# Kernel tuning notes

Measured on AMD Instinct MI355X. Metric: run time of the kernel, lower is better.

The kernel has to match this reference:

```python
import jax, jax.numpy as jnp
import numpy as np


def _dct1d_last(x, W_r, W_i):
    """DCT-II along last axis via the even/odd-reorder + FFT trick, ortho norm.

    x: [..., N] real. W_r/W_i: [1, N] rows = cos/sin(-k*pi/(2N)).
    """
    N = x.shape[-1]
    # v = [x[0], x[2], ...] ++ [x[N-1], x[N-3], ..., x[1]]  (torch index/inverted_index)
    v = jnp.concatenate([x[..., 0::2], x[..., 1::2][..., ::-1]], axis=-1)
    Vc = jnp.fft.fft(v, axis=-1)  # complex64
    V = Vc.real * W_r - Vc.imag * W_i  # [..., N]
    # ortho normalization: V[0] /= sqrt(N)*2 ; V[1:] /= sqrt(N/2)*2 ; then V *= 2
    s0 = 1.0 / (np.sqrt(N) * 2.0)
    s1 = 1.0 / (np.sqrt(N / 2.0) * 2.0)
    scale = jnp.concatenate([jnp.full((1,), s0, x.dtype), jnp.full((N - 1,), s1, x.dtype)])
    return 2.0 * V * scale


def setup_inputs() -> dict:
    key = jax.random.key(0)
    H, W = 512, 512
    x = jax.random.normal(key, (32, 3, H, W), dtype=jnp.float32)
    kw = -jnp.arange(W, dtype=jnp.float32)[None, :] * np.pi / (2 * W)
    kh = -jnp.arange(H, dtype=jnp.float32)[None, :] * np.pi / (2 * H)
    return {
        "x": x,
        "W_r_weight": jnp.cos(kw), "W_i_weight": jnp.sin(kw),
        "W_r_height": jnp.cos(kh), "W_i_height": jnp.sin(kh),
    }


def reference(x, W_r_weight, W_i_weight, W_r_height, W_i_height):
    # DCT along width (last axis)
    V = _dct1d_last(x, W_r_weight, W_i_weight)
    # transpose last two dims, DCT along height, transpose back
    V = jnp.swapaxes(V, -1, -2)
    V = _dct1d_last(V, W_r_height, W_i_height)
    return jnp.swapaxes(V, -1, -2)
```

## Files before the change

kernel.cpp:

```cpp
#include <hip/hip_runtime.h>
#include <math.h>

#define NN 512

typedef __attribute__((ext_vector_type(8))) short bf16x8;
typedef __attribute__((ext_vector_type(4))) float f32x4;
typedef __attribute__((ext_vector_type(4))) unsigned int u32x4;

__device__ inline unsigned short f2bf(float f) {
    unsigned u = __builtin_bit_cast(unsigned, f);
    u += 0x7fffu + ((u >> 16) & 1u);
    return (unsigned short)(u >> 16);
}
__device__ inline float bf2f(unsigned short h) {
    unsigned u = ((unsigned)h) << 16;
    return __builtin_bit_cast(float, u);
}
__device__ inline unsigned cvtpk_bf16(float lo, float hi) {
    unsigned r;
    asm("v_cvt_pk_bf16_f32 %0, %1, %2" : "=v"(r) : "v"(lo), "v"(hi));
    return r;
}

__global__ __launch_bounds__(256) void fill_dct_half(unsigned short* __restrict__ Ce,
                                                     unsigned short* __restrict__ Co) {
    int idx = blockIdx.x * 256 + threadIdx.x;
    int par = idx >> 16;
    int kk = (idx >> 8) & 255;
    int n = idx & 255;
    int k = 2 * kk + par;
    int m = ((2 * n + 1) * k) & 2047;
    float ang = (float)m * 3.0679615757712823e-3f;
    float s = (k == 0) ? 0.04419417382415922f : 0.0625f;
    unsigned short v = f2bf(s * cosf(ang));
    if (par) Co[kk * 256 + n] = v; else Ce[kk * 256 + n] = v;
}

#define GLB(p) ((const __attribute__((address_space(1))) unsigned int*)(const void*)(p))
#define LDS(p) ((__attribute__((address_space(3))) unsigned int*)(p))

template <int PASS>
__global__ __launch_bounds__(512, 4) void gemm_dct(const void* __restrict__ Ap,
                                                   const unsigned short* __restrict__ Ce,
                                                   const unsigned short* __restrict__ Cop,
                                                   void* __restrict__ Outp,
                                                   size_t strideIn, size_t strideOut) {
    const int nwg = (int)gridDim.x;
    const int cpx = nwg >> 3;
    const int bid = (int)blockIdx.x;
    const int nid = (bid & 7) * cpx + (bid >> 3);
    const int bx = nid & 3;
    const int by = (nid >> 2) & 3;
    const int bz = nid >> 4;

    __shared__ unsigned short sm[PASS == 1 ? 37376 : 20480];
    unsigned short* const As = sm;
    unsigned short* const Bs = sm + (PASS == 1 ? 8192 : 12288);
    unsigned short* const Rs = (PASS == 1) ? As : Bs;
    unsigned short* const Gs = (PASS == 1) ? Bs : As;
    unsigned short* const smE = sm + 20480;

    const int t = threadIdx.x;
    const int lane = t & 63;
    const int wave = t >> 6;
    const int wr = wave >> 2, wc = wave & 3;
    const int lr = lane & 15;
    const int kgx = ((lane >> 4) * 8) ^ (((lr >> 1) & 3) << 3);

    const int srow = t >> 2;
    const int sslot = t & 3;
    const int scol = (sslot ^ ((srow >> 1) & 3)) * 8;

    const int frow = t >> 2;
    const int fq = t & 3;
    const int fslot = (fq ^ ((frow >> 1) & 3)) * 8;

    const float* Xf = nullptr;
    const unsigned short* Tp = nullptr;
    const unsigned short* Gmat;
    int grow0, sgn, row0, col0;
    if constexpr (PASS == 1) {
        Xf = (const float*)Ap + (size_t)bz * strideIn;
        row0 = by * 128;
        col0 = bx * 128;
        Gmat = (bx < 2) ? Ce : Cop; grow0 = (bx & 1) * 128; sgn = (bx >= 2);
    } else {
        Tp = (const unsigned short*)Ap + (size_t)bz * strideIn;
        col0 = bx * 128;
        row0 = 0;
        Gmat = (by < 2) ? Ce : Cop; grow0 = (by & 1) * 128; sgn = (by >= 2);
    }
    const float sgnf = sgn ? -1.0f : 1.0f;

    f32x4 acc[4][2] = {};

    f32x4 rfA[2], rmA[2], rfB[2], rmB[2];
    bf16x8 gfA, gmA, gfB, gmB;

    auto stageG = [&](int buf, int k0) {
        __builtin_amdgcn_global_load_lds(GLB(Gmat + (size_t)(grow0 + srow) * 256 + k0 + scol),
                                         LDS(&Gs[buf * 4096 + srow * 32 + sslot * 8]), 16, 0, 0);
    };
    auto lr1 = [&](f32x4 (&rf)[2], f32x4 (&rm)[2], int k0) {
        const float* bfp = Xf + (size_t)(row0 + frow) * NN + k0 + fq * 8;
        const float* bmp = Xf + (size_t)(row0 + frow) * NN + (504 - k0 - fq * 8);
        rf[0] = *reinterpret_cast<const f32x4*>(bfp);
        rf[1] = *reinterpret_cast<const f32x4*>(bfp + 4);
        rm[0] = *reinterpret_cast<const f32x4*>(bmp);
        rm[1] = *reinterpret_cast<const f32x4*>(bmp + 4);
    };
    auto cw1 = [&](f32x4 (&rf)[2], f32x4 (&rm)[2], int buf) {
        unsigned p[4];
#pragma unroll
        for (int q = 0; q < 4; ++q) {
            const int j0 = 2 * q, j1 = 2 * q + 1;
            const int r0 = 7 - j0, r1 = 7 - j1;
            float s0 = fmaf(sgnf, rm[r0 >> 2][r0 & 3], rf[j0 >> 2][j0 & 3]);
            float s1 = fmaf(sgnf, rm[r1 >> 2][r1 & 3], rf[j1 >> 2][j1 & 3]);
            p[q] = cvtpk_bf16(s0, s1);
        }
        u32x4 w = {p[0], p[1], p[2], p[3]};
        *reinterpret_cast<u32x4*>(&Rs[buf * 4096 + frow * 32 + fslot]) = w;
    };
    auto lr2 = [&](bf16x8& gf, bf16x8& gm, int k0) {
        const unsigned short* bfp = Tp + (size_t)(col0 + frow) * NN + k0 + fq * 8;
        const unsigned short* bmp = Tp + (size_t)(col0 + frow) * NN + (504 - k0 - fq * 8);
        gf = *reinterpret_cast<const bf16x8*>(bfp);
        gm = *reinterpret_cast<const bf16x8*>(bmp);
    };
    auto cw2 = [&](bf16x8& gf, bf16x8& gm, int buf) {
        unsigned p[4];
#pragma unroll
        for (int q = 0; q < 4; ++q) {
            const int j0 = 2 * q, j1 = 2 * q + 1;
            float a0 = bf2f((unsigned short)gf[j0]);
            float a1 = bf2f((unsigned short)gf[j1]);
            float b0 = bf2f((unsigned short)gm[7 - j0]);
            float b1 = bf2f((unsigned short)gm[7 - j1]);
            p[q] = cvtpk_bf16(fmaf(sgnf, b0, a0), fmaf(sgnf, b1, a1));
        }
        u32x4 w = {p[0], p[1], p[2], p[3]};
        *reinterpret_cast<u32x4*>(&Rs[buf * 4096 + frow * 32 + fslot]) = w;
    };
    auto compute = [&](int kt) {
        const int rofs = (kt & 1) * 4096;
        const int gofs = (kt % 3) * 4096;
        const int aofs = (PASS == 1) ? rofs : gofs;
        const int bofs = (PASS == 1) ? gofs : rofs;
        bf16x8 a[4], b[2];
#pragma unroll
        for (int mi = 0; mi < 4; ++mi)
            a[mi] = *reinterpret_cast<const bf16x8*>(
                &As[aofs + (wr * 64 + mi * 16 + lr) * 32 + kgx]);
#pragma unroll
        for (int ni = 0; ni < 2; ++ni)
            b[ni] = *reinterpret_cast<const bf16x8*>(
                &Bs[bofs + (wc * 32 + ni * 16 + lr) * 32 + kgx]);
        __builtin_amdgcn_s_setprio(1);
#pragma unroll
        for (int mi = 0; mi < 4; ++mi)
#pragma unroll
            for (int ni = 0; ni < 2; ++ni)
                acc[mi][ni] = __builtin_amdgcn_mfma_f32_16x16x32_bf16(a[mi], b[ni],
                                                                      acc[mi][ni], 0, 0, 0);
        __builtin_amdgcn_s_setprio(0);
    };
    auto doLR = [&](int s, int k0) {
        if constexpr (PASS == 1) {
            if (s & 1) lr1(rfB, rmB, k0); else lr1(rfA, rmA, k0);
        } else {
            if (s & 1) lr2(gfB, gmB, k0); else lr2(gfA, gmA, k0);
        }
    };
    auto doCW = [&](int s) {
        const int buf = s & 1;
        if constexpr (PASS == 1) {
            if (s & 1) cw1(rfB, rmB, buf); else cw1(rfA, rmA, buf);
        } else {
            if (s & 1) cw2(gfB, gmB, buf); else cw2(gfA, gmA, buf);
        }
    };

    stageG(0, 0);
    doLR(0, 0);
    asm volatile("" ::: "memory");
    doCW(0);
    stageG(1, 32);
    asm volatile("" ::: "memory");
    doLR(1, 32);
    doLR(2, 64);
    asm volatile("s_waitcnt lgkmcnt(0)" ::: "memory");
    if constexpr (PASS == 1) asm volatile("s_waitcnt vmcnt(8)" ::: "memory");
    else                     asm volatile("s_waitcnt vmcnt(4)" ::: "memory");
    __builtin_amdgcn_s_barrier();

#pragma unroll
    for (int kt = 0; kt < 8; ++kt) {
        if (kt + 1 <= 7) doCW(kt + 1);
        if (kt + 2 <= 7) stageG((kt + 2) % 3, (kt + 2) * 32);
        asm volatile("" ::: "memory");
        if (kt + 3 <= 7) doLR(kt + 3, (kt + 3) * 32);
        compute(kt);
        asm volatile("s_waitcnt lgkmcnt(0)" ::: "memory");
        if (kt <= 4) {
            if constexpr (PASS == 1) asm volatile("s_waitcnt vmcnt(9)" ::: "memory");
            else                     asm volatile("s_waitcnt vmcnt(5)" ::: "memory");
        } else if (kt == 5) {
            if constexpr (PASS == 1) asm volatile("s_waitcnt vmcnt(5)" ::: "memory");
            else                     asm volatile("s_waitcnt vmcnt(3)" ::: "memory");
        } else if (kt == 6) {
            asm volatile("s_waitcnt vmcnt(0)" ::: "memory");
        }
        if (kt < 7) __builtin_amdgcn_s_barrier();
    }

    if constexpr (PASS == 1) {
        unsigned short* T = (unsigned short*)Outp + (size_t)bz * strideOut;
#pragma unroll
        for (int mi = 0; mi < 4; ++mi)
#pragma unroll
            for (int ni = 0; ni < 2; ++ni) {
                int gr = wr * 64 + mi * 16 + (lane >> 4) * 4;
                int gc = wc * 32 + ni * 16 + lr;
                ushort4 v;
                v.x = f2bf(acc[mi][ni][0]);
                v.y = f2bf(acc[mi][ni][1]);
                v.z = f2bf(acc[mi][ni][2]);
                v.w = f2bf(acc[mi][ni][3]);
                *reinterpret_cast<ushort4*>(&smE[gc * 132 + gr]) = v;
            }
        asm volatile("s_waitcnt lgkmcnt(0)" ::: "memory");
        __builtin_amdgcn_s_barrier();
#pragma unroll
        for (int it = 0; it < 4; ++it) {
            int gcr = wave * 16 + it * 4 + (lane >> 4);
            int physRow = (bx & 1) * 256 + 2 * gcr + (bx >> 1);
            int cb = lr * 8;
            u32x4 d = *reinterpret_cast<const u32x4*>(&smE[gcr * 132 + cb]);
            *reinterpret_cast<u32x4*>(&T[(size_t)physRow * NN + row0 + cb]) = d;
        }
    } else {
        float* O = (float*)Outp + (size_t)bz * strideOut;
#pragma unroll
        for (int mi = 0; mi < 4; ++mi)
#pragma unroll
            for (int ni = 0; ni < 2; ++ni) {
                int gc = col0 + wc * 32 + ni * 16 + lr;
#pragma unroll
                for (int rr = 0; rr < 4; ++rr) {
                    int grl = wr * 64 + mi * 16 + (lane >> 4) * 4 + rr;
                    int ih = (by & 1) * 128 + grl;
                    int q = 2 * ih + (by >> 1);
                    O[(size_t)q * NN + gc] = acc[mi][ni][rr];
                }
            }
    }
}

extern "C" void kernel_launch(void* const* d_in, const int* in_sizes, int n_in,
                              void* d_out, int out_size, void* d_ws, size_t ws_size,
                              hipStream_t stream) {
    const float* x = (const float*)d_in[0];
    float* out = (float*)d_out;

    const int imgs = in_sizes[0] / (NN * NN);
    const size_t imgElems = (size_t)NN * NN;
    const size_t imgB16 = imgElems * 2;

    unsigned short* Ce = (unsigned short*)d_ws;
    unsigned short* Co = Ce + 65536;
    unsigned short* Tb = Co + 65536;

    long long budget = (long long)ws_size - 262144;
    int maxchunk = (int)(budget / (long long)imgB16);
    if (maxchunk < 1) maxchunk = 1;
    if (maxchunk > imgs) maxchunk = imgs;

    hipLaunchKernelGGL(fill_dct_half, dim3(512), dim3(256), 0, stream, Ce, Co);

    for (int i0 = 0; i0 < imgs; i0 += maxchunk) {
        int c = imgs - i0 < maxchunk ? imgs - i0 : maxchunk;
        hipLaunchKernelGGL((gemm_dct<1>), dim3(16 * c), dim3(512), 0, stream,
                           x + (size_t)i0 * imgElems, Ce, Co, Tb, imgElems, imgElems);
        hipLaunchKernelGGL((gemm_dct<2>), dim3(16 * c), dim3(512), 0, stream,
                           Tb, Ce, Co, out + (size_t)i0 * imgElems, imgElems, imgElems);
    }
}
```

Measured before the change: 74.77 us.

## Enlarge GEMM tiles to 128x256 per block and halve the grid

Each workgroup now computes a 128x256 output tile: it stages a full 256-row half of the DCT basis (even or odd parity) and fuses the parity into the block index. Each wave moves from a 4x2 to a 4x4 MFMA accumulator grid, so more math is done per LDS fragment load. Every block now serves both 128-column halves of its parity, so the fold of the input row is loaded and formed once instead of twice. The register prefetch depth drops from two stages to one and the wait counts are adjusted to match. The costs are more accumulator registers, a larger LDS footprint that may reduce occupancy, half as many blocks for the GPU to spread across its compute units, and less latency hiding on the global loads.

```diff
diff --git a/kernel.cpp b/kernel.cpp
--- a/kernel.cpp
+++ b/kernel.cpp
@@ -49,23 +49,21 @@
     const int cpx = nwg >> 3;
     const int bid = (int)blockIdx.x;
     const int nid = (bid & 7) * cpx + (bid >> 3);
-    const int bx = nid & 3;
-    const int by = (nid >> 2) & 3;
-    const int bz = nid >> 4;
-
-    __shared__ unsigned short sm[PASS == 1 ? 37376 : 20480];
-    unsigned short* const As = sm;
-    unsigned short* const Bs = sm + (PASS == 1 ? 8192 : 12288);
-    unsigned short* const Rs = (PASS == 1) ? As : Bs;
-    unsigned short* const Gs = (PASS == 1) ? Bs : As;
-    unsigned short* const smE = sm + 20480;
+    const int par = nid & 1;
+    const int bq = (nid >> 1) & 3;
+    const int bz = nid >> 3;
+
+    __shared__ unsigned short sm[PASS == 1 ? 33792 : 32768];
+    unsigned short* const Rs = (PASS == 1) ? sm : sm + 24576;
+    unsigned short* const Gs = (PASS == 1) ? sm + 8192 : sm;
 
     const int t = threadIdx.x;
     const int lane = t & 63;
     const int wave = t >> 6;
-    const int wr = wave >> 2, wc = wave & 3;
     const int lr = lane & 15;
     const int kgx = ((lane >> 4) * 8) ^ (((lr >> 1) & 3) << 3);
+    const int AW = (PASS == 1) ? (wave >> 2) : (wave >> 1);
+    const int BW = (PASS == 1) ? (wave & 3) : (wave & 1);
 
     const int srow = t >> 2;
     const int sslot = t & 3;
@@ -77,137 +75,120 @@
 
     const float* Xf = nullptr;
     const unsigned short* Tp = nullptr;
-    const unsigned short* Gmat;
-    int grow0, sgn, row0, col0;
+    const unsigned short* const Gmat = par ? Cop : Ce;
+    const float sgnf = par ? -1.0f : 1.0f;
+    int row0 = 0, col0 = 0;
     if constexpr (PASS == 1) {
         Xf = (const float*)Ap + (size_t)bz * strideIn;
-        row0 = by * 128;
-        col0 = bx * 128;
-        Gmat = (bx < 2) ? Ce : Cop; grow0 = (bx & 1) * 128; sgn = (bx >= 2);
+        row0 = bq * 128;
     } else {
         Tp = (const unsigned short*)Ap + (size_t)bz * strideIn;
-        col0 = bx * 128;
-        row0 = 0;
-        Gmat = (by < 2) ? Ce : Cop; grow0 = (by & 1) * 128; sgn = (by >= 2);
-    }
-    const float sgnf = sgn ? -1.0f : 1.0f;
-
-    f32x4 acc[4][2] = {};
-
-    f32x4 rfA[2], rmA[2], rfB[2], rmB[2];
-    bf16x8 gfA, gmA, gfB, gmB;
+        col0 = bq * 128;
+    }
+
+    f32x4 acc[4][4] = {};
+
+    f32x4 rf[2], rm[2];
+    bf16x8 gf, gm;
 
     auto stageG = [&](int buf, int k0) {
-        __builtin_amdgcn_global_load_lds(GLB(Gmat + (size_t)(grow0 + srow) * 256 + k0 + scol),
-                                         LDS(&Gs[buf * 4096 + srow * 32 + sslot * 8]), 16, 0, 0);
-    };
-    auto lr1 = [&](f32x4 (&rf)[2], f32x4 (&rm)[2], int k0) {
-        const float* bfp = Xf + (size_t)(row0 + frow) * NN + k0 + fq * 8;
-        const float* bmp = Xf + (size_t)(row0 + frow) * NN + (504 - k0 - fq * 8);
-        rf[0] = *reinterpret_cast<const f32x4*>(bfp);
-        rf[1] = *reinterpret_cast<const f32x4*>(bfp + 4);
-        rm[0] = *reinterpret_cast<const f32x4*>(bmp);
-        rm[1] = *reinterpret_cast<const f32x4*>(bmp + 4);
-    };
-    auto cw1 = [&](f32x4 (&rf)[2], f32x4 (&rm)[2], int buf) {
+        __builtin_amdgcn_global_load_lds(GLB(Gmat + (size_t)srow * 256 + k0 + scol),
+                                         LDS(&Gs[buf * 8192 + srow * 32 + sslot * 8]), 16, 0, 0);
+        __builtin_amdgcn_global_load_lds(GLB(Gmat + (size_t)(128 + srow) * 256 + k0 + scol),
+                                         LDS(&Gs[buf * 8192 + (128 + srow) * 32 + sslot * 8]), 16, 0, 0);
+    };
+    auto doLR = [&](int k0) {
+        if constexpr (PASS == 1) {
+            const float* bfp = Xf + (size_t)(row0 + frow) * NN + k0 + fq * 8;
+            const float* bmp = Xf + (size_t)(row0 + frow) * NN + (504 - k0 - fq * 8);
+            rf[0] = *reinterpret_cast<const f32x4*>(bfp);
+            rf[1] = *reinterpret_cast<const f32x4*>(bfp + 4);
+            rm[0] = *reinterpret_cast<const f32x4*>(bmp);
+            rm[1] = *reinterpret_cast<const f32x4*>(bmp + 4);
+        } else {
+            const unsigned short* bfp = Tp + (size_t)(col0 + frow) * NN + k0 + fq * 8;
+            const unsigned short* bmp = Tp + (size_t)(col0 + frow) * NN + (504 - k0 - fq * 8);
+            gf = *reinterpret_cast<const bf16x8*>(bfp);
+            gm = *reinterpret_cast<const bf16x8*>(bmp);
+        }
+    };
+    auto doCW = [&](int s) {
+        const int buf = s & 1;
         unsigned p[4];
-#pragma unroll
-        for (int q = 0; q < 4; ++q) {
-            const int j0 = 2 * q, j1 = 2 * q + 1;
-            const int r0 = 7 - j0, r1 = 7 - j1;
-            float s0 = fmaf(sgnf, rm[r0 >> 2][r0 & 3], rf[j0 >> 2][j0 & 3]);
-            float s1 = fmaf(sgnf, rm[r1 >> 2][r1 & 3], rf[j1 >> 2][j1 & 3]);
-            p[q] = cvtpk_bf16(s0, s1);
+        if constexpr (PASS == 1) {
+#pragma unroll
+            for (int q = 0; q < 4; ++q) {
+                const int j0 = 2 * q, j1 = 2 * q + 1;
+                const int r0 = 7 - j0, r1 = 7 - j1;
+                float s0 = fmaf(sgnf, rm[r0 >> 2][r0 & 3], rf[j0 >> 2][j0 & 3]);
+                float s1 = fmaf(sgnf, rm[r1 >> 2][r1 & 3], rf[j1 >> 2][j1 & 3]);
+                p[q] = cvtpk_bf16(s0, s1);
+            }
+        } else {
+#pragma unroll
+            for (int q = 0; q < 4; ++q) {
+                const int j0 = 2 * q, j1 = 2 * q + 1;
+                float a0 = bf2f((unsigned short)gf[j0]);
+                float a1 = bf2f((unsigned short)gf[j1]);
+                float b0 = bf2f((unsigned short)gm[7 - j0]);
+                float b1 = bf2f((unsigned short)gm[7 - j1]);
+                p[q] = cvtpk_bf16(fmaf(sgnf, b0, a0), fmaf(sgnf, b1, a1));
+            }
         }
         u32x4 w = {p[0], p[1], p[2], p[3]};
         *reinterpret_cast<u32x4*>(&Rs[buf * 4096 + frow * 32 + fslot]) = w;
     };
-    auto lr2 = [&](bf16x8& gf, bf16x8& gm, int k0) {
-        const unsigned short* bfp = Tp + (size_t)(col0 + frow) * NN + k0 + fq * 8;
-        const unsigned short* bmp = Tp + (size_t)(col0 + frow) * NN + (504 - k0 - fq * 8);
-        gf = *reinterpret_cast<const bf16x8*>(bfp);
-        gm = *reinterpret_cast<const bf16x8*>(bmp);
-    };
-    auto cw2 = [&](bf16x8& gf, bf16x8& gm, int buf) {
-        unsigned p[4];
-#pragma unroll
-        for (int q = 0; q < 4; ++q) {
-            const int j0 = 2 * q, j1 = 2 * q + 1;
-            float a0 = bf2f((unsigned short)gf[j0]);
-            float a1 = bf2f((unsigned short)gf[j1]);
-            float b0 = bf2f((unsigned short)gm[7 - j0]);
-            float b1 = bf2f((unsigned short)gm[7 - j1]);
-            p[q] = cvtpk_bf16(fmaf(sgnf, b0, a0), fmaf(sgnf, b1, a1));
-        }
-        u32x4 w = {p[0], p[1], p[2], p[3]};
-        *reinterpret_cast<u32x4*>(&Rs[buf * 4096 + frow * 32 + fslot]) = w;
-    };
     auto compute = [&](int kt) {
         const int rofs = (kt & 1) * 4096;
-        const int gofs = (kt % 3) * 4096;
+        const int gofs = (kt % 3) * 8192;
+        const unsigned short* const Aside = (PASS == 1) ? Rs : Gs;
+        const unsigned short* const Bside = (PASS == 1) ? Gs : Rs;
         const int aofs = (PASS == 1) ? rofs : gofs;
         const int bofs = (PASS == 1) ? gofs : rofs;
-        bf16x8 a[4], b[2];
+        bf16x8 a[4], b[4];
 #pragma unroll
         for (int mi = 0; mi < 4; ++mi)
             a[mi] = *reinterpret_cast<const bf16x8*>(
-                &As[aofs + (wr * 64 + mi * 16 + lr) * 32 + kgx]);
-#pragma unroll
-        for (int ni = 0; ni < 2; ++ni)
+                &Aside[aofs + (AW * 64 + mi * 16 + lr) * 32 + kgx]);
+#pragma unroll
+        for (int ni = 0; ni < 4; ++ni)
             b[ni] = *reinterpret_cast<const bf16x8*>(
-                &Bs[bofs + (wc * 32 + ni * 16 + lr) * 32 + kgx]);
+                &Bside[bofs + (BW * 64 + ni * 16 + lr) * 32 + kgx]);
         __builtin_amdgcn_s_setprio(1);
 #pragma unroll
         for (int mi = 0; mi < 4; ++mi)
 #pragma unroll
-            for (int ni = 0; ni < 2; ++ni)
+            for (int ni = 0; ni < 4; ++ni)
                 acc[mi][ni] = __builtin_amdgcn_mfma_f32_16x16x32_bf16(a[mi], b[ni],
                                                                       acc[mi][ni], 0, 0, 0);
         __builtin_amdgcn_s_setprio(0);
     };
-    auto doLR = [&](int s, int k0) {
-        if constexpr (PASS == 1) {
-            if (s & 1) lr1(rfB, rmB, k0); else lr1(rfA, rmA, k0);
-        } else {
-            if (s & 1) lr2(gfB, gmB, k0); else lr2(gfA, gmA, k0);
-        }
-    };
-    auto doCW = [&](int s) {
-        const int buf = s & 1;
-        if constexpr (PASS == 1) {
-            if (s & 1) cw1(rfB, rmB, buf); else cw1(rfA, rmA, buf);
-        } else {
-            if (s & 1) cw2(gfB, gmB, buf); else cw2(gfA, gmA, buf);
-        }
-    };
 
     stageG(0, 0);
-    doLR(0, 0);
+    doLR(0);
     asm volatile("" ::: "memory");
     doCW(0);
     stageG(1, 32);
     asm volatile("" ::: "memory");
-    doLR(1, 32);
-    doLR(2, 64);
+    doLR(32);
     asm volatile("s_waitcnt lgkmcnt(0)" ::: "memory");
-    if constexpr (PASS == 1) asm volatile("s_waitcnt vmcnt(8)" ::: "memory");
+    if constexpr (PASS == 1) asm volatile("s_waitcnt vmcnt(6)" ::: "memory");
     else                     asm volatile("s_waitcnt vmcnt(4)" ::: "memory");
     __builtin_amdgcn_s_barrier();
 
 #pragma unroll
     for (int kt = 0; kt < 8; ++kt) {
         if (kt + 1 <= 7) doCW(kt + 1);
-        if (kt + 2 <= 7) stageG((kt + 2) % 3, (kt + 2) * 32);
-        asm volatile("" ::: "memory");
-        if (kt + 3 <= 7) doLR(kt + 3, (kt + 3) * 32);
+        if (kt + 2 <= 7) {
+            stageG((kt + 2) % 3, (kt + 2) * 32);
+            asm volatile("" ::: "memory");
+            doLR((kt + 2) * 32);
+        }
         compute(kt);
         asm volatile("s_waitcnt lgkmcnt(0)" ::: "memory");
-        if (kt <= 4) {
-            if constexpr (PASS == 1) asm volatile("s_waitcnt vmcnt(9)" ::: "memory");
-            else                     asm volatile("s_waitcnt vmcnt(5)" ::: "memory");
-        } else if (kt == 5) {
-            if constexpr (PASS == 1) asm volatile("s_waitcnt vmcnt(5)" ::: "memory");
-            else                     asm volatile("s_waitcnt vmcnt(3)" ::: "memory");
+        if (kt <= 5) {
+            if constexpr (PASS == 1) asm volatile("s_waitcnt vmcnt(6)" ::: "memory");
+            else                     asm volatile("s_waitcnt vmcnt(4)" ::: "memory");
         } else if (kt == 6) {
             asm volatile("s_waitcnt vmcnt(0)" ::: "memory");
         }
@@ -216,27 +197,28 @@
 
     if constexpr (PASS == 1) {
         unsigned short* T = (unsigned short*)Outp + (size_t)bz * strideOut;
-#pragma unroll
-        for (int mi = 0; mi < 4; ++mi)
-#pragma unroll
-            for (int ni = 0; ni < 2; ++ni) {
-                int gr = wr * 64 + mi * 16 + (lane >> 4) * 4;
-                int gc = wc * 32 + ni * 16 + lr;
+        __builtin_amdgcn_s_barrier();
+#pragma unroll
+        for (int mi = 0; mi < 4; ++mi)
+#pragma unroll
+            for (int ni = 0; ni < 4; ++ni) {
+                int gr = AW * 64 + mi * 16 + (lane >> 4) * 4;
+                int gc = BW * 64 + ni * 16 + lr;
                 ushort4 v;
                 v.x = f2bf(acc[mi][ni][0]);
                 v.y = f2bf(acc[mi][ni][1]);
                 v.z = f2bf(acc[mi][ni][2]);
                 v.w = f2bf(acc[mi][ni][3]);
-                *reinterpret_cast<ushort4*>(&smE[gc * 132 + gr]) = v;
+                *reinterpret_cast<ushort4*>(&sm[gc * 132 + gr]) = v;
             }
         asm volatile("s_waitcnt lgkmcnt(0)" ::: "memory");
         __builtin_amdgcn_s_barrier();
 #pragma unroll
-        for (int it = 0; it < 4; ++it) {
-            int gcr = wave * 16 + it * 4 + (lane >> 4);
-            int physRow = (bx & 1) * 256 + 2 * gcr + (bx >> 1);
-            int cb = lr * 8;
-            u32x4 d = *reinterpret_cast<const u32x4*>(&smE[gcr * 132 + cb]);
+        for (int it = 0; it < 8; ++it) {
+            int gcr = it * 32 + (t >> 4);
+            int physRow = 2 * gcr + par;
+            int cb = (t & 15) * 8;
+            u32x4 d = *reinterpret_cast<const u32x4*>(&sm[gcr * 132 + cb]);
             *reinterpret_cast<u32x4*>(&T[(size_t)physRow * NN + row0 + cb]) = d;
         }
     } else {
@@ -244,13 +226,12 @@
 #pragma unroll
         for (int mi = 0; mi < 4; ++mi)
 #pragma unroll
-            for (int ni = 0; ni < 2; ++ni) {
-                int gc = col0 + wc * 32 + ni * 16 + lr;
+            for (int ni = 0; ni < 4; ++ni) {
+                int gc = col0 + BW * 64 + ni * 16 + lr;
 #pragma unroll
                 for (int rr = 0; rr < 4; ++rr) {
-                    int grl = wr * 64 + mi * 16 + (lane >> 4) * 4 + rr;
-                    int ih = (by & 1) * 128 + grl;
-                    int q = 2 * ih + (by >> 1);
+                    int qp = AW * 64 + mi * 16 + (lane >> 4) * 4 + rr;
+                    int q = 2 * qp + par;
                     O[(size_t)q * NN + gc] = acc[mi][ni][rr];
                 }
             }
@@ -280,9 +261,9 @@
 
     for (int i0 = 0; i0 < imgs; i0 += maxchunk) {
         int c = imgs - i0 < maxchunk ? imgs - i0 : maxchunk;
-        hipLaunchKernelGGL((gemm_dct<1>), dim3(16 * c), dim3(512), 0, stream,
+        hipLaunchKernelGGL((gemm_dct<1>), dim3(8 * c), dim3(512), 0, stream,
                            x + (size_t)i0 * imgElems, Ce, Co, Tb, imgElems, imgElems);
-        hipLaunchKernelGGL((gemm_dct<2>), dim3(16 * c), dim3(512), 0, stream,
+        hipLaunchKernelGGL((gemm_dct<2>), dim3(8 * c), dim3(512), 0, stream,
                            Tb, Ce, Co, out + (size_t)i0 * imgElems, imgElems, imgElems);
     }
 }
```

After: 79.04 us. +5.7%, slower.

## Double K-tile depth to 64 and shorten pipeline to four stages

Applied to the files above, without the earlier changes.

Each pipeline step now covers a K-chunk of 64 instead of 32, so the main loop runs 4 iterations instead of 8, with half as many barriers, and the G/R LDS buffers are doubled in size. The fine-grained vmcnt waits are removed and the epilogue staging buffer is aliased onto the start of the shared array, guarded by an extra barrier. The aim is to cut per-iteration synchronisation overhead. In exchange the kernel uses more LDS (80 KB versus about 73 KB or 40 KB per pass) and more prefetch registers, which may lower occupancy, and the prefetch distance is now shorter relative to compute.

```diff
diff --git a/kernel.cpp b/kernel.cpp
--- a/kernel.cpp
+++ b/kernel.cpp
@@ -53,17 +53,15 @@
     const int by = (nid >> 2) & 3;
     const int bz = nid >> 4;
 
-    __shared__ unsigned short sm[PASS == 1 ? 37376 : 20480];
-    unsigned short* const As = sm;
-    unsigned short* const Bs = sm + (PASS == 1 ? 8192 : 12288);
-    unsigned short* const Rs = (PASS == 1) ? As : Bs;
-    unsigned short* const Gs = (PASS == 1) ? Bs : As;
-    unsigned short* const smE = sm + 20480;
+    __shared__ unsigned short sm[40960];
+    unsigned short* const Rs = (PASS == 1) ? sm : sm + 24576;
+    unsigned short* const Gs = (PASS == 1) ? sm + 16384 : sm;
 
     const int t = threadIdx.x;
     const int lane = t & 63;
     const int wave = t >> 6;
-    const int wr = wave >> 2, wc = wave & 3;
+    const int wr = wave >> 2;
+    const int wc = wave & 3;
     const int lr = lane & 15;
     const int kgx = ((lane >> 4) * 8) ^ (((lr >> 1) & 3) << 3);
 
@@ -94,128 +92,119 @@
 
     f32x4 acc[4][2] = {};
 
-    f32x4 rfA[2], rmA[2], rfB[2], rmB[2];
-    bf16x8 gfA, gmA, gfB, gmB;
+    f32x4 rf[2][2], rm[2][2];
+    bf16x8 gf[2], gm[2];
 
     auto stageG = [&](int buf, int k0) {
-        __builtin_amdgcn_global_load_lds(GLB(Gmat + (size_t)(grow0 + srow) * 256 + k0 + scol),
-                                         LDS(&Gs[buf * 4096 + srow * 32 + sslot * 8]), 16, 0, 0);
-    };
-    auto lr1 = [&](f32x4 (&rf)[2], f32x4 (&rm)[2], int k0) {
-        const float* bfp = Xf + (size_t)(row0 + frow) * NN + k0 + fq * 8;
-        const float* bmp = Xf + (size_t)(row0 + frow) * NN + (504 - k0 - fq * 8);
-        rf[0] = *reinterpret_cast<const f32x4*>(bfp);
-        rf[1] = *reinterpret_cast<const f32x4*>(bfp + 4);
-        rm[0] = *reinterpret_cast<const f32x4*>(bmp);
-        rm[1] = *reinterpret_cast<const f32x4*>(bmp + 4);
-    };
-    auto cw1 = [&](f32x4 (&rf)[2], f32x4 (&rm)[2], int buf) {
-        unsigned p[4];
-#pragma unroll
-        for (int q = 0; q < 4; ++q) {
-            const int j0 = 2 * q, j1 = 2 * q + 1;
-            const int r0 = 7 - j0, r1 = 7 - j1;
-            float s0 = fmaf(sgnf, rm[r0 >> 2][r0 & 3], rf[j0 >> 2][j0 & 3]);
-            float s1 = fmaf(sgnf, rm[r1 >> 2][r1 & 3], rf[j1 >> 2][j1 & 3]);
-            p[q] = cvtpk_bf16(s0, s1);
-        }
-        u32x4 w = {p[0], p[1], p[2], p[3]};
-        *reinterpret_cast<u32x4*>(&Rs[buf * 4096 + frow * 32 + fslot]) = w;
-    };
-    auto lr2 = [&](bf16x8& gf, bf16x8& gm, int k0) {
-        const unsigned short* bfp = Tp + (size_t)(col0 + frow) * NN + k0 + fq * 8;
-        const unsigned short* bmp = Tp + (size_t)(col0 + frow) * NN + (504 - k0 - fq * 8);
-        gf = *reinterpret_cast<const bf16x8*>(bfp);
-        gm = *reinterpret_cast<const bf16x8*>(bmp);
-    };
-    auto cw2 = [&](bf16x8& gf, bf16x8& gm, int buf) {
-        unsigned p[4];
-#pragma unroll
-        for (int q = 0; q < 4; ++q) {
-            const int j0 = 2 * q, j1 = 2 * q + 1;
-            float a0 = bf2f((unsigned short)gf[j0]);
-            float a1 = bf2f((unsigned short)gf[j1]);
-            float b0 = bf2f((unsigned short)gm[7 - j0]);
-            float b1 = bf2f((unsigned short)gm[7 - j1]);
-            p[q] = cvtpk_bf16(fmaf(sgnf, b0, a0), fmaf(sgnf, b1, a1));
-        }
-        u32x4 w = {p[0], p[1], p[2], p[3]};
-        *reinterpret_cast<u32x4*>(&Rs[buf * 4096 + frow * 32 + fslot]) = w;
+#pragma unroll
+        for (int h = 0; h < 2; ++h)
+            __builtin_amdgcn_global_load_lds(
+                GLB(Gmat + (size_t)(grow0 + srow) * 256 + k0 + h * 32 + scol),
+                LDS(&Gs[buf * 8192 + h * 4096 + srow * 32 + sslot * 8]), 16, 0, 0);
+    };
+    auto doLR = [&](int k0) {
+        if constexpr (PASS == 1) {
+#pragma unroll
+            for (int h = 0; h < 2; ++h) {
+                const float* bfp = Xf + (size_t)(row0 + frow) * NN + k0 + h * 32 + fq * 8;
+                const float* bmp = Xf + (size_t)(row0 + frow) * NN + (504 - k0 - h * 32 - fq * 8);
+                rf[h][0] = *reinterpret_cast<const f32x4*>(bfp);
+                rf[h][1] = *reinterpret_cast<const f32x4*>(bfp + 4);
+                rm[h][0] = *reinterpret_cast<const f32x4*>(bmp);
+                rm[h][1] = *reinterpret_cast<const f32x4*>(bmp + 4);
+            }
+        } else {
+#pragma unroll
+            for (int h = 0; h < 2; ++h) {
+                const unsigned short* bfp = Tp + (size_t)(col0 + frow) * NN + k0 + h * 32 + fq * 8;
+                const unsigned short* bmp = Tp + (size_t)(col0 + frow) * NN + (504 - k0 - h * 32 - fq * 8);
+                gf[h] = *reinterpret_cast<const bf16x8*>(bfp);
+                gm[h] = *reinterpret_cast<const bf16x8*>(bmp);
+            }
+        }
+    };
+    auto doCW = [&](int s) {
+        const int buf = s & 1;
+#pragma unroll
+        for (int h = 0; h < 2; ++h) {
+            unsigned p[4];
+            if constexpr (PASS == 1) {
+#pragma unroll
+                for (int q = 0; q < 4; ++q) {
+                    const int j0 = 2 * q, j1 = 2 * q + 1;
+                    const int r0 = 7 - j0, r1 = 7 - j1;
+                    float s0 = fmaf(sgnf, rm[h][r0 >> 2][r0 & 3], rf[h][j0 >> 2][j0 & 3]);
+                    float s1 = fmaf(sgnf, rm[h][r1 >> 2][r1 & 3], rf[h][j1 >> 2][j1 & 3]);
+                    p[q] = cvtpk_bf16(s0, s1);
+                }
+            } else {
+#pragma unroll
+                for (int q = 0; q < 4; ++q) {
+                    const int j0 = 2 * q, j1 = 2 * q + 1;
+                    float a0 = bf2f((unsigned short)gf[h][j0]);
+                    float a1 = bf2f((unsigned short)gf[h][j1]);
+                    float b0 = bf2f((unsigned short)gm[h][7 - j0]);
+                    float b1 = bf2f((unsigned short)gm[h][7 - j1]);
+                    p[q] = cvtpk_bf16(fmaf(sgnf, b0, a0), fmaf(sgnf, b1, a1));
+                }
+            }
+            u32x4 w = {p[0], p[1], p[2], p[3]};
+            *reinterpret_cast<u32x4*>(&Rs[buf * 8192 + h * 4096 + frow * 32 + fslot]) = w;
+        }
     };
     auto compute = [&](int kt) {
-        const int rofs = (kt & 1) * 4096;
-        const int gofs = (kt % 3) * 4096;
+        const int rofs = (kt & 1) * 8192;
+        const int gofs = (kt % 3) * 8192;
+        const unsigned short* const Aside = (PASS == 1) ? Rs : Gs;
+        const unsigned short* const Bside = (PASS == 1) ? Gs : Rs;
         const int aofs = (PASS == 1) ? rofs : gofs;
         const int bofs = (PASS == 1) ? gofs : rofs;
-        bf16x8 a[4], b[2];
-#pragma unroll
-        for (int mi = 0; mi < 4; ++mi)
-            a[mi] = *reinterpret_cast<const bf16x8*>(
-                &As[aofs + (wr * 64 + mi * 16 + lr) * 32 + kgx]);
-#pragma unroll
-        for (int ni = 0; ni < 2; ++ni)
-            b[ni] = *reinterpret_cast<const bf16x8*>(
-                &Bs[bofs + (wc * 32 + ni * 16 + lr) * 32 + kgx]);
-        __builtin_amdgcn_s_setprio(1);
-#pragma unroll
-        for (int mi = 0; mi < 4; ++mi)
+#pragma unroll
+        for (int ks = 0; ks < 2; ++ks) {
+            const int ho = ks * 4096;
+            bf16x8 a[4], b[2];
+#pragma unroll
+            for (int mi = 0; mi < 4; ++mi)
+                a[mi] = *reinterpret_cast<const bf16x8*>(
+                    &Aside[aofs + ho + (wr * 64 + mi * 16 + lr) * 32 + kgx]);
 #pragma unroll
             for (int ni = 0; ni < 2; ++ni)
-                acc[mi][ni] = __builtin_amdgcn_mfma_f32_16x16x32_bf16(a[mi], b[ni],
-                                                                      acc[mi][ni], 0, 0, 0);
-        __builtin_amdgcn_s_setprio(0);
-    };
-    auto doLR = [&](int s, int k0) {
-        if constexpr (PASS == 1) {
-            if (s & 1) lr1(rfB, rmB, k0); else lr1(rfA, rmA, k0);
-        } else {
-            if (s & 1) lr2(gfB, gmB, k0); else lr2(gfA, gmA, k0);
-        }
-    };
-    auto doCW = [&](int s) {
-        const int buf = s & 1;
-        if constexpr (PASS == 1) {
-            if (s & 1) cw1(rfB, rmB, buf); else cw1(rfA, rmA, buf);
-        } else {
-            if (s & 1) cw2(gfB, gmB, buf); else cw2(gfA, gmA, buf);
+                b[ni] = *reinterpret_cast<const bf16x8*>(
+                    &Bside[bofs + ho + (wc * 32 + ni * 16 + lr) * 32 + kgx]);
+            __builtin_amdgcn_s_setprio(1);
+#pragma unroll
+            for (int mi = 0; mi < 4; ++mi)
+#pragma unroll
+                for (int ni = 0; ni < 2; ++ni)
+                    acc[mi][ni] = __builtin_amdgcn_mfma_f32_16x16x32_bf16(a[mi], b[ni],
+                                                                          acc[mi][ni], 0, 0, 0);
+            __builtin_amdgcn_s_setprio(0);
         }
     };
 
     stageG(0, 0);
-    doLR(0, 0);
+    stageG(1, 64);
     asm volatile("" ::: "memory");
+    doLR(0);
     doCW(0);
-    stageG(1, 32);
-    asm volatile("" ::: "memory");
-    doLR(1, 32);
-    doLR(2, 64);
+    doLR(64);
     asm volatile("s_waitcnt lgkmcnt(0)" ::: "memory");
-    if constexpr (PASS == 1) asm volatile("s_waitcnt vmcnt(8)" ::: "memory");
-    else                     asm volatile("s_waitcnt vmcnt(4)" ::: "memory");
     __builtin_amdgcn_s_barrier();
 
 #pragma unroll
-    for (int kt = 0; kt < 8; ++kt) {
-        if (kt + 1 <= 7) doCW(kt + 1);
-        if (kt + 2 <= 7) stageG((kt + 2) % 3, (kt + 2) * 32);
+    for (int kt = 0; kt < 4; ++kt) {
+        if (kt + 2 <= 3) stageG((kt + 2) % 3, (kt + 2) * 64);
         asm volatile("" ::: "memory");
-        if (kt + 3 <= 7) doLR(kt + 3, (kt + 3) * 32);
+        if (kt + 1 <= 3) doCW(kt + 1);
+        if (kt + 2 <= 3) doLR((kt + 2) * 64);
         compute(kt);
         asm volatile("s_waitcnt lgkmcnt(0)" ::: "memory");
-        if (kt <= 4) {
-            if constexpr (PASS == 1) asm volatile("s_waitcnt vmcnt(9)" ::: "memory");
-            else                     asm volatile("s_waitcnt vmcnt(5)" ::: "memory");
-        } else if (kt == 5) {
-            if constexpr (PASS == 1) asm volatile("s_waitcnt vmcnt(5)" ::: "memory");
-            else                     asm volatile("s_waitcnt vmcnt(3)" ::: "memory");
-        } else if (kt == 6) {
-            asm volatile("s_waitcnt vmcnt(0)" ::: "memory");
-        }
-        if (kt < 7) __builtin_amdgcn_s_barrier();
+        if (kt < 3) __builtin_amdgcn_s_barrier();
     }
 
     if constexpr (PASS == 1) {
         unsigned short* T = (unsigned short*)Outp + (size_t)bz * strideOut;
+        __builtin_amdgcn_s_barrier();
 #pragma unroll
         for (int mi = 0; mi < 4; ++mi)
 #pragma unroll
@@ -227,7 +216,7 @@
                 v.y = f2bf(acc[mi][ni][1]);
                 v.z = f2bf(acc[mi][ni][2]);
                 v.w = f2bf(acc[mi][ni][3]);
-                *reinterpret_cast<ushort4*>(&smE[gc * 132 + gr]) = v;
+                *reinterpret_cast<ushort4*>(&sm[gc * 132 + gr]) = v;
             }
         asm volatile("s_waitcnt lgkmcnt(0)" ::: "memory");
         __builtin_amdgcn_s_barrier();
@@ -236,7 +225,7 @@
             int gcr = wave * 16 + it * 4 + (lane >> 4);
             int physRow = (bx & 1) * 256 + 2 * gcr + (bx >> 1);
             int cb = lr * 8;
-            u32x4 d = *reinterpret_cast<const u32x4*>(&smE[gcr * 132 + cb]);
+            u32x4 d = *reinterpret_cast<const u32x4*>(&sm[gcr * 132 + cb]);
             *reinterpret_cast<u32x4*>(&T[(size_t)physRow * NN + row0 + cb]) = d;
         }
     } else {
```

Measured after the change: 69.10 us. -7.6%, faster.
